# Optimization experiments

Hardware: AMD Instinct MI355X
Metric: run time of the kernel (lower is better)

Reference implementation:

```python
import jax, jax.numpy as jnp
import numpy as np

B, D, ATT, C = 256, 2048, 512, 1024
TEMP = 4.0  # cfg.JS_Softmax_Temp
SCALE = 20.0
N_GROUPS = 32


def setup_inputs() -> dict:
    key = jax.random.key(0)
    k1, k2, k3, k4 = jax.random.split(key, 4)
    x = jax.random.normal(k1, (B, D), dtype=jnp.float32)
    gt_s_labels = jax.random.randint(k2, (B,), 0, N_GROUPS)
    W = jax.random.normal(k3, (ATT, D), dtype=jnp.float32) * 0.02  # Linear weight [out,in]
    b = jnp.zeros((ATT,), dtype=jnp.float32)
    seen_att = jax.random.normal(k4, (C, ATT), dtype=jnp.float32)
    return {"x": x, "gt_s_labels": gt_s_labels, "W": W, "b": b, "seen_att": seen_att}


def _l2norm(v):
    return v / jnp.maximum(jnp.linalg.norm(v, axis=-1, keepdims=True), 1e-12)


def _adv_loss(x, W, b, seen_att, labels):
    # GRL is identity in forward; classifier = Linear(D, ATT)
    y_att = _l2norm(x @ W.T + b)            # [B, ATT]
    sa = _l2norm(seen_att)                   # [C, ATT]
    logits = SCALE * (y_att @ sa.T)          # [B, C]
    logP = jax.nn.log_softmax(logits / TEMP, axis=-1)
    P = jnp.exp(logP)                        # [B, C] softmax distributions
    # Pairwise mixture log((p_i + p_j)/2): [B, B, C]
    logM = jnp.log((P[:, None, :] + P[None, :, :]) * 0.5)
    negH = jnp.sum(P * logP, axis=-1)        # [B], = -entropy_i
    cross = jnp.einsum('ic,ijc->ij', P, logM)  # sum_c p_i log m_ij
    A = negH[:, None] - cross                # KL(p_i || m_ij), [B, B]
    JS = 0.5 * (A + A.T)                     # m symmetric => JS_ij
    idx = jnp.arange(B)
    mask = (labels[:, None] == labels[None, :]) & (idx[None, :] > idx[:, None])
    cnt = jnp.sum(mask)
    loss = jnp.where(cnt == 0, jnp.float32(0.0),
                     jnp.sum(jnp.where(mask, JS, 0.0)) / jnp.maximum(cnt, 1).astype(jnp.float32))
    return loss * (TEMP ** 2)


def reference(x, gt_s_labels, W, b, seen_att):
    return _adv_loss(x, W, b, seen_att, gt_s_labels)
```

## Files before the change

kernel.cpp:

```cpp
#include <hip/hip_runtime.h>
#include <math.h>

static constexpr int Bn  = 256;
static constexpr int Dd  = 2048;
static constexpr int ATT = 512;
static constexpr int Cc  = 1024;
static constexpr int SK1 = 16;
static constexpr int SK2 = 8;
static constexpr int BM = 128, BN = 64, BK = 32;
static constexpr int APITCH = BK + 8;

typedef __attribute__((ext_vector_type(8))) short short8v;
typedef __attribute__((ext_vector_type(4))) float f32x4;

__device__ __forceinline__ float wave_reduce_sum(float v) {
#pragma unroll
    for (int off = 32; off; off >>= 1) v += __shfl_down(v, off, 64);
    return v;
}
__device__ __forceinline__ float wave_reduce_max(float v) {
#pragma unroll
    for (int off = 32; off; off >>= 1) v = fmaxf(v, __shfl_down(v, off, 64));
    return v;
}
__device__ __forceinline__ float block_reduce_sum(float v) {
    __shared__ float sm_s[4];
    v = wave_reduce_sum(v);
    __syncthreads();
    if ((threadIdx.x & 63) == 0) sm_s[threadIdx.x >> 6] = v;
    __syncthreads();
    return sm_s[0] + sm_s[1] + sm_s[2] + sm_s[3];
}
__device__ __forceinline__ float block_reduce_max(float v) {
    __shared__ float sm_m[4];
    v = wave_reduce_max(v);
    __syncthreads();
    if ((threadIdx.x & 63) == 0) sm_m[threadIdx.x >> 6] = v;
    __syncthreads();
    return fmaxf(fmaxf(sm_m[0], sm_m[1]), fmaxf(sm_m[2], sm_m[3]));
}

__device__ __forceinline__ void splitbf(float v, unsigned short& h, unsigned short& l) {
    const unsigned int b = __float_as_uint(v);
    h = (unsigned short)(b >> 16);
    const float r = v - __uint_as_float(b & 0xFFFF0000u);
    l = (unsigned short)(__float_as_uint(r) >> 16);
}
__device__ __forceinline__ void stage4(const float4 v, unsigned short* hi,
                                       unsigned short* lo, int off) {
    unsigned short h0, h1, h2, h3, l0, l1, l2, l3;
    splitbf(v.x, h0, l0); splitbf(v.y, h1, l1);
    splitbf(v.z, h2, l2); splitbf(v.w, h3, l3);
    *(ushort4*)(hi + off) = make_ushort4(h0, h1, h2, h3);
    *(ushort4*)(lo + off) = make_ushort4(l0, l1, l2, l3);
}

__device__ __forceinline__ void gemm_tile_mfma(const float* __restrict__ A,
                                               const float* __restrict__ B,
                                               float* __restrict__ dst, int N, int K,
                                               int row0, int col0, int kbase, int kc,
                                               unsigned short* __restrict__ Ahi,
                                               unsigned short* __restrict__ Alo,
                                               unsigned short* __restrict__ Bhi,
                                               unsigned short* __restrict__ Blo) {
    constexpr int FA = BK / 4;
    constexpr int NA = BM * FA / 256;
    constexpr int NB = BN * FA / 256;
    const int tid = threadIdx.x;
    const int lane = tid & 63, wv = tid >> 6;
    const int fr = lane & 15, fg = lane >> 4;

    float4 pa[NA], pb[NB];
#pragma unroll
    for (int u = 0; u < NA; ++u) {
        const int t = tid + u * 256, r = t / FA, c4 = (t % FA) * 4;
        pa[u] = *(const float4*)(A + (size_t)(row0 + r) * K + kbase + c4);
    }
#pragma unroll
    for (int u = 0; u < NB; ++u) {
        const int t = tid + u * 256, r = t / FA, c4 = (t % FA) * 4;
        pb[u] = *(const float4*)(B + (size_t)(col0 + r) * K + kbase + c4);
    }
    f32x4 acc[2][4] = {};
    for (int k0 = kbase; k0 < kbase + kc; k0 += BK) {
        __syncthreads();
#pragma unroll
        for (int u = 0; u < NA; ++u) {
            const int t = tid + u * 256, r = t / FA, c4 = (t % FA) * 4;
            stage4(pa[u], Ahi, Alo, r * APITCH + c4);
        }
#pragma unroll
        for (int u = 0; u < NB; ++u) {
            const int t = tid + u * 256, r = t / FA, c4 = (t % FA) * 4;
            stage4(pb[u], Bhi, Blo, r * APITCH + c4);
        }
        __syncthreads();
        if (k0 + BK < kbase + kc) {
            const int kn = k0 + BK;
#pragma unroll
            for (int u = 0; u < NA; ++u) {
                const int t = tid + u * 256, r = t / FA, c4 = (t % FA) * 4;
                pa[u] = *(const float4*)(A + (size_t)(row0 + r) * K + kn + c4);
            }
#pragma unroll
            for (int u = 0; u < NB; ++u) {
                const int t = tid + u * 256, r = t / FA, c4 = (t % FA) * 4;
                pb[u] = *(const float4*)(B + (size_t)(col0 + r) * K + kn + c4);
            }
        }
        short8v ah[2], al[2];
#pragma unroll
        for (int im = 0; im < 2; ++im) {
            const int mrow = (wv * 2 + im) * 16 + fr;
            ah[im] = *(short8v*)(Ahi + mrow * APITCH + fg * 8);
            al[im] = *(short8v*)(Alo + mrow * APITCH + fg * 8);
        }
#pragma unroll
        for (int in = 0; in < 4; ++in) {
            const int nrow = in * 16 + fr;
            const short8v bh = *(short8v*)(Bhi + nrow * APITCH + fg * 8);
            const short8v bl = *(short8v*)(Blo + nrow * APITCH + fg * 8);
#pragma unroll
            for (int im = 0; im < 2; ++im) {
                acc[im][in] = __builtin_amdgcn_mfma_f32_16x16x32_bf16(ah[im], bh, acc[im][in], 0, 0, 0);
                acc[im][in] = __builtin_amdgcn_mfma_f32_16x16x32_bf16(ah[im], bl, acc[im][in], 0, 0, 0);
                acc[im][in] = __builtin_amdgcn_mfma_f32_16x16x32_bf16(al[im], bh, acc[im][in], 0, 0, 0);
            }
        }
    }
#pragma unroll
    for (int im = 0; im < 2; ++im) {
#pragma unroll
        for (int in = 0; in < 4; ++in) {
#pragma unroll
            for (int r = 0; r < 4; ++r) {
                const int m = row0 + (wv * 2 + im) * 16 + fg * 4 + r;
                const int c = col0 + in * 16 + fr;
                dst[(size_t)m * N + c] = acc[im][in][r];
            }
        }
    }
}

__global__ __launch_bounds__(256, 2) void k1_gemm1_sanorm(const float* __restrict__ x,
                                                          const float* __restrict__ W,
                                                          const float* __restrict__ seen,
                                                          float* __restrict__ part,
                                                          float* __restrict__ sa,
                                                          int* __restrict__ doneCnt) {
    __shared__ unsigned short AhiS[BM * APITCH];
    __shared__ unsigned short AloS[BM * APITCH];
    __shared__ unsigned short BhiS[BN * APITCH];
    __shared__ unsigned short BloS[BN * APITCH];
    const int bid = blockIdx.x, tid = threadIdx.x;
    if (bid < 256) {
        const int bx = bid & 7, by = (bid >> 3) & 1, bz = bid >> 4;
        gemm_tile_mfma(x, W, part + (size_t)bz * Bn * ATT, ATT, Dd,
                       by * BM, bx * BN, bz * (Dd / SK1), Dd / SK1,
                       AhiS, AloS, BhiS, BloS);
    } else {
        if (bid == 256 && tid == 0) *doneCnt = 0;
#pragma unroll
        for (int u = 0; u < 4; ++u) {
            const int r = (bid - 256) * 4 + u, c = tid * 2;
            const float2 v = *(const float2*)(seen + (size_t)r * ATT + c);
            float ss = block_reduce_sum(fmaf(v.x, v.x, v.y * v.y));
            const float sc = 1.0f / fmaxf(sqrtf(ss), 1e-12f);
            *(float2*)(sa + (size_t)r * ATT + c) = make_float2(v.x * sc, v.y * sc);
        }
    }
}

__global__ __launch_bounds__(256) void k2_yanorm(const float* __restrict__ part,
                                                 const float* __restrict__ bias,
                                                 float* __restrict__ ya) {
    const int m = blockIdx.x, c = threadIdx.x * 2;
    float2 s = *(const float2*)(bias + c);
#pragma unroll
    for (int z = 0; z < SK1; ++z) {
        const float2 p = *(const float2*)(part + (size_t)z * Bn * ATT + (size_t)m * ATT + c);
        s.x += p.x; s.y += p.y;
    }
    float ss = block_reduce_sum(fmaf(s.x, s.x, s.y * s.y));
    const float sc = 1.0f / fmaxf(sqrtf(ss), 1e-12f);
    *(float2*)(ya + (size_t)m * ATT + c) = make_float2(s.x * sc, s.y * sc);
}

__global__ __launch_bounds__(256, 2) void k3_gemm2(const float* __restrict__ ya,
                                                   const float* __restrict__ sa,
                                                   float* __restrict__ part) {
    __shared__ unsigned short AhiS[BM * APITCH];
    __shared__ unsigned short AloS[BM * APITCH];
    __shared__ unsigned short BhiS[BN * APITCH];
    __shared__ unsigned short BloS[BN * APITCH];
    const int bid = blockIdx.x;
    const int bx = bid & 15, by = (bid >> 4) & 1, bz = bid >> 5;
    gemm_tile_mfma(ya, sa, part + (size_t)bz * Bn * Cc, Cc, ATT,
                   by * BM, bx * BN, bz * (ATT / SK2), ATT / SK2,
                   AhiS, AloS, BhiS, BloS);
}

__global__ __launch_bounds__(256) void k4_softmax(const float* __restrict__ part,
                                                  float* __restrict__ P,
                                                  float* __restrict__ negH) {
    const int i = blockIdx.x, c = threadIdx.x * 4;
    float4 a = make_float4(0.f, 0.f, 0.f, 0.f);
#pragma unroll
    for (int z = 0; z < SK2; ++z) {
        const float4 p = *(const float4*)(part + (size_t)z * Bn * Cc + (size_t)i * Cc + c);
        a.x += p.x; a.y += p.y; a.z += p.z; a.w += p.w;
    }
    float lv[4] = {a.x * 5.0f, a.y * 5.0f, a.z * 5.0f, a.w * 5.0f};
    float lm = fmaxf(fmaxf(lv[0], lv[1]), fmaxf(lv[2], lv[3]));
    lm = block_reduce_max(lm);
    float se = 0.f;
#pragma unroll
    for (int k = 0; k < 4; ++k) se += __expf(lv[k] - lm);
    se = block_reduce_sum(se);
    const float logZ = __logf(se);
    float nh = 0.f;
    float4 pv;
#pragma unroll
    for (int k = 0; k < 4; ++k) {
        const float lp = lv[k] - lm - logZ;
        const float p = __expf(lp);
        (&pv.x)[k] = p;
        nh = fmaf(p, lp, nh);
    }
    *(float4*)(P + (size_t)i * Cc + c) = pv;
    nh = block_reduce_sum(nh);
    if (threadIdx.x == 0) negH[i] = nh;
}

__global__ __launch_bounds__(256) void k5_pairjs_fin(const float* __restrict__ P,
                                                     const float* __restrict__ negH,
                                                     const int* __restrict__ labels,
                                                     float* __restrict__ pairSum,
                                                     float* __restrict__ pairCnt,
                                                     int* __restrict__ doneCnt,
                                                     float* __restrict__ out) {
    const int i = blockIdx.x, tid = threadIdx.x;
    __shared__ int lbl[Bn];
    __shared__ float nh_s[Bn];
    __shared__ int isLast;
    lbl[tid] = labels[tid];
    nh_s[tid] = negH[tid];
    __syncthreads();
    const int li = lbl[i];
    const float4 pi = *(const float4*)(P + (size_t)i * Cc + tid * 4);
    const float nhi = nh_s[i];

    float tsum = 0.f;
    float nsum = 0.f, cnt = 0.f;
    for (int j = i + 1; j < Bn; ++j) {
        if (lbl[j] != li) continue;
        const float4 pj = *(const float4*)(P + (size_t)j * Cc + tid * 4);
        float t;
        t = pi.x + pj.x; tsum = fmaf(t, __logf(0.5f * t), tsum);
        t = pi.y + pj.y; tsum = fmaf(t, __logf(0.5f * t), tsum);
        t = pi.z + pj.z; tsum = fmaf(t, __logf(0.5f * t), tsum);
        t = pi.w + pj.w; tsum = fmaf(t, __logf(0.5f * t), tsum);
        if (tid == 0) { nsum += nhi + nh_s[j]; cnt += 1.0f; }
    }
    const float s = block_reduce_sum(tsum);
    if (tid == 0) {
        pairSum[i] = 0.5f * (nsum - s);
        pairCnt[i] = cnt;
        __threadfence();
        isLast = (atomicAdd(doneCnt, 1) == Bn - 1);
    }
    __syncthreads();
    if (isLast) {
        __threadfence();
        float fs = block_reduce_sum(pairSum[tid]);
        __syncthreads();
        const float fc = block_reduce_sum(pairCnt[tid]);
        if (tid == 0) out[0] = (fc == 0.0f) ? 0.0f : (fs / fc) * 16.0f;
    }
}

extern "C" void kernel_launch(void* const* d_in, const int* in_sizes, int n_in,
                              void* d_out, int out_size, void* d_ws, size_t ws_size,
                              hipStream_t stream) {
    const float* x      = (const float*)d_in[0];
    const int*   labels = (const int*)d_in[1];
    const float* W      = (const float*)d_in[2];
    const float* bias   = (const float*)d_in[3];
    const float* seen   = (const float*)d_in[4];
    float* out = (float*)d_out;

    char* ws = (char*)d_ws;
    float* part    = (float*)(ws);
    float* sa      = (float*)(ws + (8u << 20));
    float* ya      = (float*)(ws + (10u << 20));
    float* P       = (float*)(ws + (10u << 20) + (512u << 10));
    float* negH    = (float*)(ws + (11u << 20) + (512u << 10));
    float* pairSum = negH + Bn;
    float* pairCnt = pairSum + Bn;
    int*   doneCnt = (int*)(pairCnt + Bn);

    k1_gemm1_sanorm<<<512, 256, 0, stream>>>(x, W, seen, part, sa, doneCnt);
    k2_yanorm<<<Bn, 256, 0, stream>>>(part, bias, ya);
    k3_gemm2<<<256, 256, 0, stream>>>(ya, sa, part);
    k4_softmax<<<Bn, 256, 0, stream>>>(part, P, negH);
    k5_pairjs_fin<<<Bn, 256, 0, stream>>>(P, negH, labels, pairSum, pairCnt, doneCnt, out);
}
```

Measured before the change: 51.39 us.

## Pre-split GEMM operands into bf16 hi/lo arrays and halve split-K factors

Adds a separate kernel that splits x and W into bf16 high and low halves once in global memory. The normalization kernels now write bf16 hi/lo pairs directly, so the GEMM tiles load ready-made bf16 data with 16-byte loads instead of converting fp32 inside every tile. Split-K factors are halved, which shrinks the grids and the partial-sum traffic but gives each block a longer K loop. The trade-off is an extra kernel launch and an extra pass over x and W to produce the split copies.

Result: slower. 55.85 us (+8.7%).

```diff
diff --git a/kernel.cpp b/kernel.cpp
--- a/kernel.cpp
+++ b/kernel.cpp
@@ -5,10 +5,10 @@
 static constexpr int Dd  = 2048;
 static constexpr int ATT = 512;
 static constexpr int Cc  = 1024;
-static constexpr int SK1 = 16;
-static constexpr int SK2 = 8;
+static constexpr int SK1 = 8;
+static constexpr int SK2 = 4;
 static constexpr int BM = 128, BN = 64, BK = 32;
-static constexpr int APITCH = BK + 8;
+static constexpr int AP = 40;
 
 typedef __attribute__((ext_vector_type(8))) short short8v;
 typedef __attribute__((ext_vector_type(4))) float f32x4;
@@ -46,80 +46,76 @@
     const float r = v - __uint_as_float(b & 0xFFFF0000u);
     l = (unsigned short)(__float_as_uint(r) >> 16);
 }
-__device__ __forceinline__ void stage4(const float4 v, unsigned short* hi,
-                                       unsigned short* lo, int off) {
+
+__global__ __launch_bounds__(256) void k0_split(const float* __restrict__ x,
+                                                const float* __restrict__ W,
+                                                unsigned short* __restrict__ xh,
+                                                unsigned short* __restrict__ xl,
+                                                unsigned short* __restrict__ wh,
+                                                unsigned short* __restrict__ wl) {
+    const float* src; unsigned short *dh, *dl; int idx;
+    if (blockIdx.x < 512) {
+        src = x; dh = xh; dl = xl; idx = blockIdx.x * 256 + threadIdx.x;
+    } else {
+        src = W; dh = wh; dl = wl; idx = (blockIdx.x - 512) * 256 + threadIdx.x;
+    }
+    const float4 v = ((const float4*)src)[idx];
     unsigned short h0, h1, h2, h3, l0, l1, l2, l3;
     splitbf(v.x, h0, l0); splitbf(v.y, h1, l1);
     splitbf(v.z, h2, l2); splitbf(v.w, h3, l3);
-    *(ushort4*)(hi + off) = make_ushort4(h0, h1, h2, h3);
-    *(ushort4*)(lo + off) = make_ushort4(l0, l1, l2, l3);
-}
-
-__device__ __forceinline__ void gemm_tile_mfma(const float* __restrict__ A,
-                                               const float* __restrict__ B,
-                                               float* __restrict__ dst, int N, int K,
-                                               int row0, int col0, int kbase, int kc,
-                                               unsigned short* __restrict__ Ahi,
-                                               unsigned short* __restrict__ Alo,
-                                               unsigned short* __restrict__ Bhi,
-                                               unsigned short* __restrict__ Blo) {
-    constexpr int FA = BK / 4;
-    constexpr int NA = BM * FA / 256;
-    constexpr int NB = BN * FA / 256;
+    *(ushort4*)(dh + (size_t)idx * 4) = make_ushort4(h0, h1, h2, h3);
+    *(ushort4*)(dl + (size_t)idx * 4) = make_ushort4(l0, l1, l2, l3);
+}
+
+__device__ __forceinline__ void gemm_tile_bf(const unsigned short* __restrict__ Ah,
+                                             const unsigned short* __restrict__ Al,
+                                             const unsigned short* __restrict__ Bh,
+                                             const unsigned short* __restrict__ Bl,
+                                             float* __restrict__ dst, int N, int K,
+                                             int row0, int col0, int kbase, int kc,
+                                             unsigned short* __restrict__ LAh,
+                                             unsigned short* __restrict__ LAl,
+                                             unsigned short* __restrict__ LBh,
+                                             unsigned short* __restrict__ LBl) {
     const int tid = threadIdx.x;
     const int lane = tid & 63, wv = tid >> 6;
     const int fr = lane & 15, fg = lane >> 4;
-
-    float4 pa[NA], pb[NB];
-#pragma unroll
-    for (int u = 0; u < NA; ++u) {
-        const int t = tid + u * 256, r = t / FA, c4 = (t % FA) * 4;
-        pa[u] = *(const float4*)(A + (size_t)(row0 + r) * K + kbase + c4);
-    }
-#pragma unroll
-    for (int u = 0; u < NB; ++u) {
-        const int t = tid + u * 256, r = t / FA, c4 = (t % FA) * 4;
-        pb[u] = *(const float4*)(B + (size_t)(col0 + r) * K + kbase + c4);
-    }
+    const int ar = tid >> 2, ac8 = (tid & 3) * 8;
+
+    short8v pah0, pah1, pal0, pal1, pbh0, pbl0;
+    #define LDG(p, r, kk) (*(const short8v*)((p) + (size_t)(r) * K + (kk)))
+    pah0 = LDG(Ah, row0 + ar, kbase + ac8);  pah1 = LDG(Ah, row0 + 64 + ar, kbase + ac8);
+    pal0 = LDG(Al, row0 + ar, kbase + ac8);  pal1 = LDG(Al, row0 + 64 + ar, kbase + ac8);
+    pbh0 = LDG(Bh, col0 + ar, kbase + ac8);  pbl0 = LDG(Bl, col0 + ar, kbase + ac8);
+
     f32x4 acc[2][4] = {};
     for (int k0 = kbase; k0 < kbase + kc; k0 += BK) {
         __syncthreads();
-#pragma unroll
-        for (int u = 0; u < NA; ++u) {
-            const int t = tid + u * 256, r = t / FA, c4 = (t % FA) * 4;
-            stage4(pa[u], Ahi, Alo, r * APITCH + c4);
-        }
-#pragma unroll
-        for (int u = 0; u < NB; ++u) {
-            const int t = tid + u * 256, r = t / FA, c4 = (t % FA) * 4;
-            stage4(pb[u], Bhi, Blo, r * APITCH + c4);
-        }
+        *(short8v*)(LAh + ar * AP + ac8) = pah0;
+        *(short8v*)(LAh + (64 + ar) * AP + ac8) = pah1;
+        *(short8v*)(LAl + ar * AP + ac8) = pal0;
+        *(short8v*)(LAl + (64 + ar) * AP + ac8) = pal1;
+        *(short8v*)(LBh + ar * AP + ac8) = pbh0;
+        *(short8v*)(LBl + ar * AP + ac8) = pbl0;
         __syncthreads();
         if (k0 + BK < kbase + kc) {
-            const int kn = k0 + BK;
-#pragma unroll
-            for (int u = 0; u < NA; ++u) {
-                const int t = tid + u * 256, r = t / FA, c4 = (t % FA) * 4;
-                pa[u] = *(const float4*)(A + (size_t)(row0 + r) * K + kn + c4);
-            }
-#pragma unroll
-            for (int u = 0; u < NB; ++u) {
-                const int t = tid + u * 256, r = t / FA, c4 = (t % FA) * 4;
-                pb[u] = *(const float4*)(B + (size_t)(col0 + r) * K + kn + c4);
-            }
+            const int kn = k0 + BK + ac8;
+            pah0 = LDG(Ah, row0 + ar, kn);  pah1 = LDG(Ah, row0 + 64 + ar, kn);
+            pal0 = LDG(Al, row0 + ar, kn);  pal1 = LDG(Al, row0 + 64 + ar, kn);
+            pbh0 = LDG(Bh, col0 + ar, kn);  pbl0 = LDG(Bl, col0 + ar, kn);
         }
         short8v ah[2], al[2];
 #pragma unroll
         for (int im = 0; im < 2; ++im) {
             const int mrow = (wv * 2 + im) * 16 + fr;
-            ah[im] = *(short8v*)(Ahi + mrow * APITCH + fg * 8);
-            al[im] = *(short8v*)(Alo + mrow * APITCH + fg * 8);
+            ah[im] = *(short8v*)(LAh + mrow * AP + fg * 8);
+            al[im] = *(short8v*)(LAl + mrow * AP + fg * 8);
         }
 #pragma unroll
         for (int in = 0; in < 4; ++in) {
             const int nrow = in * 16 + fr;
-            const short8v bh = *(short8v*)(Bhi + nrow * APITCH + fg * 8);
-            const short8v bl = *(short8v*)(Blo + nrow * APITCH + fg * 8);
+            const short8v bh = *(short8v*)(LBh + nrow * AP + fg * 8);
+            const short8v bl = *(short8v*)(LBl + nrow * AP + fg * 8);
 #pragma unroll
             for (int im = 0; im < 2; ++im) {
                 acc[im][in] = __builtin_amdgcn_mfma_f32_16x16x32_bf16(ah[im], bh, acc[im][in], 0, 0, 0);
@@ -128,52 +124,55 @@
             }
         }
     }
-#pragma unroll
-    for (int im = 0; im < 2; ++im) {
-#pragma unroll
-        for (int in = 0; in < 4; ++in) {
+    #undef LDG
+#pragma unroll
+    for (int im = 0; im < 2; ++im)
+#pragma unroll
+        for (int in = 0; in < 4; ++in)
 #pragma unroll
             for (int r = 0; r < 4; ++r) {
                 const int m = row0 + (wv * 2 + im) * 16 + fg * 4 + r;
                 const int c = col0 + in * 16 + fr;
                 dst[(size_t)m * N + c] = acc[im][in][r];
             }
-        }
-    }
-}
-
-__global__ __launch_bounds__(256, 2) void k1_gemm1_sanorm(const float* __restrict__ x,
-                                                          const float* __restrict__ W,
+}
+
+__global__ __launch_bounds__(256, 2) void k1_gemm1_sanorm(const unsigned short* __restrict__ xh,
+                                                          const unsigned short* __restrict__ xl,
+                                                          const unsigned short* __restrict__ wh,
+                                                          const unsigned short* __restrict__ wl,
                                                           const float* __restrict__ seen,
                                                           float* __restrict__ part,
-                                                          float* __restrict__ sa,
+                                                          unsigned short* __restrict__ sah,
+                                                          unsigned short* __restrict__ sal,
                                                           int* __restrict__ doneCnt) {
-    __shared__ unsigned short AhiS[BM * APITCH];
-    __shared__ unsigned short AloS[BM * APITCH];
-    __shared__ unsigned short BhiS[BN * APITCH];
-    __shared__ unsigned short BloS[BN * APITCH];
+    __shared__ unsigned short LAh[BM * AP], LAl[BM * AP];
+    __shared__ unsigned short LBh[BN * AP], LBl[BN * AP];
     const int bid = blockIdx.x, tid = threadIdx.x;
-    if (bid < 256) {
+    if (bid < 128) {
         const int bx = bid & 7, by = (bid >> 3) & 1, bz = bid >> 4;
-        gemm_tile_mfma(x, W, part + (size_t)bz * Bn * ATT, ATT, Dd,
-                       by * BM, bx * BN, bz * (Dd / SK1), Dd / SK1,
-                       AhiS, AloS, BhiS, BloS);
+        gemm_tile_bf(xh, xl, wh, wl, part + (size_t)bz * Bn * ATT, ATT, Dd,
+                     by * BM, bx * BN, bz * (Dd / SK1), Dd / SK1, LAh, LAl, LBh, LBl);
     } else {
-        if (bid == 256 && tid == 0) *doneCnt = 0;
+        if (bid == 128 && tid == 0) *doneCnt = 0;
 #pragma unroll
         for (int u = 0; u < 4; ++u) {
-            const int r = (bid - 256) * 4 + u, c = tid * 2;
+            const int r = (bid - 128) * 4 + u, c = tid * 2;
             const float2 v = *(const float2*)(seen + (size_t)r * ATT + c);
             float ss = block_reduce_sum(fmaf(v.x, v.x, v.y * v.y));
             const float sc = 1.0f / fmaxf(sqrtf(ss), 1e-12f);
-            *(float2*)(sa + (size_t)r * ATT + c) = make_float2(v.x * sc, v.y * sc);
+            unsigned short h0, h1, l0, l1;
+            splitbf(v.x * sc, h0, l0); splitbf(v.y * sc, h1, l1);
+            *(ushort2*)(sah + (size_t)r * ATT + c) = make_ushort2(h0, h1);
+            *(ushort2*)(sal + (size_t)r * ATT + c) = make_ushort2(l0, l1);
         }
     }
 }
 
 __global__ __launch_bounds__(256) void k2_yanorm(const float* __restrict__ part,
                                                  const float* __restrict__ bias,
-                                                 float* __restrict__ ya) {
+                                                 unsigned short* __restrict__ yah,
+                                                 unsigned short* __restrict__ yal) {
     const int m = blockIdx.x, c = threadIdx.x * 2;
     float2 s = *(const float2*)(bias + c);
 #pragma unroll
@@ -183,21 +182,23 @@
     }
     float ss = block_reduce_sum(fmaf(s.x, s.x, s.y * s.y));
     const float sc = 1.0f / fmaxf(sqrtf(ss), 1e-12f);
-    *(float2*)(ya + (size_t)m * ATT + c) = make_float2(s.x * sc, s.y * sc);
-}
-
-__global__ __launch_bounds__(256, 2) void k3_gemm2(const float* __restrict__ ya,
-                                                   const float* __restrict__ sa,
+    unsigned short h0, h1, l0, l1;
+    splitbf(s.x * sc, h0, l0); splitbf(s.y * sc, h1, l1);
+    *(ushort2*)(yah + (size_t)m * ATT + c) = make_ushort2(h0, h1);
+    *(ushort2*)(yal + (size_t)m * ATT + c) = make_ushort2(l0, l1);
+}
+
+__global__ __launch_bounds__(256, 2) void k3_gemm2(const unsigned short* __restrict__ yah,
+                                                   const unsigned short* __restrict__ yal,
+                                                   const unsigned short* __restrict__ sah,
+                                                   const unsigned short* __restrict__ sal,
                                                    float* __restrict__ part) {
-    __shared__ unsigned short AhiS[BM * APITCH];
-    __shared__ unsigned short AloS[BM * APITCH];
-    __shared__ unsigned short BhiS[BN * APITCH];
-    __shared__ unsigned short BloS[BN * APITCH];
+    __shared__ unsigned short LAh[BM * AP], LAl[BM * AP];
+    __shared__ unsigned short LBh[BN * AP], LBl[BN * AP];
     const int bid = blockIdx.x;
     const int bx = bid & 15, by = (bid >> 4) & 1, bz = bid >> 5;
-    gemm_tile_mfma(ya, sa, part + (size_t)bz * Bn * Cc, Cc, ATT,
-                   by * BM, bx * BN, bz * (ATT / SK2), ATT / SK2,
-                   AhiS, AloS, BhiS, BloS);
+    gemm_tile_bf(yah, yal, sah, sal, part + (size_t)bz * Bn * Cc, Cc, ATT,
+                 by * BM, bx * BN, bz * (ATT / SK2), ATT / SK2, LAh, LAl, LBh, LBl);
 }
 
 __global__ __launch_bounds__(256) void k4_softmax(const float* __restrict__ part,
@@ -290,18 +291,25 @@
     float* out = (float*)d_out;
 
     char* ws = (char*)d_ws;
-    float* part    = (float*)(ws);
-    float* sa      = (float*)(ws + (8u << 20));
-    float* ya      = (float*)(ws + (10u << 20));
-    float* P       = (float*)(ws + (10u << 20) + (512u << 10));
-    float* negH    = (float*)(ws + (11u << 20) + (512u << 10));
+    float*          part = (float*)(ws);
+    unsigned short* xh   = (unsigned short*)(ws + (4u << 20));
+    unsigned short* xl   = (unsigned short*)(ws + (5u << 20));
+    unsigned short* wh   = (unsigned short*)(ws + (6u << 20));
+    unsigned short* wl   = (unsigned short*)(ws + (8u << 20));
+    unsigned short* sah  = (unsigned short*)(ws + (10u << 20));
+    unsigned short* sal  = (unsigned short*)(ws + (11u << 20));
+    unsigned short* yah  = (unsigned short*)(ws + (12u << 20));
+    unsigned short* yal  = (unsigned short*)(ws + (12u << 20) + (256u << 10));
+    float*          P    = (float*)(ws + (13u << 20));
+    float*          negH = (float*)(ws + (14u << 20));
     float* pairSum = negH + Bn;
     float* pairCnt = pairSum + Bn;
     int*   doneCnt = (int*)(pairCnt + Bn);
 
-    k1_gemm1_sanorm<<<512, 256, 0, stream>>>(x, W, seen, part, sa, doneCnt);
-    k2_yanorm<<<Bn, 256, 0, stream>>>(part, bias, ya);
-    k3_gemm2<<<256, 256, 0, stream>>>(ya, sa, part);
+    k0_split<<<1536, 256, 0, stream>>>(x, W, xh, xl, wh, wl);
+    k1_gemm1_sanorm<<<384, 256, 0, stream>>>(xh, xl, wh, wl, seen, part, sah, sal, doneCnt);
+    k2_yanorm<<<Bn, 256, 0, stream>>>(part, bias, yah, yal);
+    k3_gemm2<<<128, 256, 0, stream>>>(yah, yal, sah, sal, part);
     k4_softmax<<<Bn, 256, 0, stream>>>(part, P, negH);
     k5_pairjs_fin<<<Bn, 256, 0, stream>>>(P, negH, labels, pairSum, pairCnt, doneCnt, out);
 }
```

## Fuse y-norm into GEMM1 and softmax into pair-JS via grid-wide spin barriers

Applied to the files above, without the earlier changes.

Removes two kernel launches. The y_att normalization now runs in the sa-norm blocks of the first kernel after they spin on a counter bumped by the GEMM tiles. Softmax now runs at the start of the pair-JS kernel, followed by a grid-wide atomic barrier. A hipMemsetAsync resets the counters each call. This cuts launch gaps between stages, but it depends on all blocks being co-resident to avoid deadlock and adds a memset plus spin-wait overhead.

New measurement: 156.0 us. 204% more time.

```diff
diff --git a/kernel.cpp b/kernel.cpp
--- a/kernel.cpp
+++ b/kernel.cpp
@@ -8,7 +8,7 @@
 static constexpr int SK1 = 16;
 static constexpr int SK2 = 8;
 static constexpr int BM = 128, BN = 64, BK = 32;
-static constexpr int APITCH = BK + 8;
+static constexpr int APITCH = 40;
 
 typedef __attribute__((ext_vector_type(8))) short short8v;
 typedef __attribute__((ext_vector_type(4))) float f32x4;
@@ -38,6 +38,19 @@
     if ((threadIdx.x & 63) == 0) sm_m[threadIdx.x >> 6] = v;
     __syncthreads();
     return fmaxf(fmaxf(sm_m[0], sm_m[1]), fmaxf(sm_m[2], sm_m[3]));
+}
+
+__device__ __forceinline__ void signal_done(int* cnt) {
+    __threadfence();
+    if (threadIdx.x == 0) atomicAdd(cnt, 1);
+}
+__device__ __forceinline__ void wait_for(int* cnt, int target) {
+    if (threadIdx.x == 0) {
+        while (__hip_atomic_load(cnt, __ATOMIC_ACQUIRE, __HIP_MEMORY_SCOPE_AGENT) < target)
+            __builtin_amdgcn_s_sleep(2);
+    }
+    __syncthreads();
+    __threadfence();
 }
 
 __device__ __forceinline__ void splitbf(float v, unsigned short& h, unsigned short& l) {
@@ -129,25 +142,25 @@
         }
     }
 #pragma unroll
-    for (int im = 0; im < 2; ++im) {
-#pragma unroll
-        for (int in = 0; in < 4; ++in) {
+    for (int im = 0; im < 2; ++im)
+#pragma unroll
+        for (int in = 0; in < 4; ++in)
 #pragma unroll
             for (int r = 0; r < 4; ++r) {
                 const int m = row0 + (wv * 2 + im) * 16 + fg * 4 + r;
                 const int c = col0 + in * 16 + fr;
                 dst[(size_t)m * N + c] = acc[im][in][r];
             }
-        }
-    }
-}
-
-__global__ __launch_bounds__(256, 2) void k1_gemm1_sanorm(const float* __restrict__ x,
-                                                          const float* __restrict__ W,
-                                                          const float* __restrict__ seen,
-                                                          float* __restrict__ part,
-                                                          float* __restrict__ sa,
-                                                          int* __restrict__ doneCnt) {
+}
+
+__global__ __launch_bounds__(256, 2) void k1_gemm1_norms(const float* __restrict__ x,
+                                                         const float* __restrict__ W,
+                                                         const float* __restrict__ seen,
+                                                         const float* __restrict__ bias,
+                                                         float* __restrict__ part,
+                                                         float* __restrict__ sa,
+                                                         float* __restrict__ ya,
+                                                         int* __restrict__ g1done) {
     __shared__ unsigned short AhiS[BM * APITCH];
     __shared__ unsigned short AloS[BM * APITCH];
     __shared__ unsigned short BhiS[BN * APITCH];
@@ -158,8 +171,9 @@
         gemm_tile_mfma(x, W, part + (size_t)bz * Bn * ATT, ATT, Dd,
                        by * BM, bx * BN, bz * (Dd / SK1), Dd / SK1,
                        AhiS, AloS, BhiS, BloS);
+        __syncthreads();
+        signal_done(g1done);
     } else {
-        if (bid == 256 && tid == 0) *doneCnt = 0;
 #pragma unroll
         for (int u = 0; u < 4; ++u) {
             const int r = (bid - 256) * 4 + u, c = tid * 2;
@@ -168,22 +182,18 @@
             const float sc = 1.0f / fmaxf(sqrtf(ss), 1e-12f);
             *(float2*)(sa + (size_t)r * ATT + c) = make_float2(v.x * sc, v.y * sc);
         }
-    }
-}
-
-__global__ __launch_bounds__(256) void k2_yanorm(const float* __restrict__ part,
-                                                 const float* __restrict__ bias,
-                                                 float* __restrict__ ya) {
-    const int m = blockIdx.x, c = threadIdx.x * 2;
-    float2 s = *(const float2*)(bias + c);
-#pragma unroll
-    for (int z = 0; z < SK1; ++z) {
-        const float2 p = *(const float2*)(part + (size_t)z * Bn * ATT + (size_t)m * ATT + c);
-        s.x += p.x; s.y += p.y;
-    }
-    float ss = block_reduce_sum(fmaf(s.x, s.x, s.y * s.y));
-    const float sc = 1.0f / fmaxf(sqrtf(ss), 1e-12f);
-    *(float2*)(ya + (size_t)m * ATT + c) = make_float2(s.x * sc, s.y * sc);
+        wait_for(g1done, 256);
+        const int m = bid - 256, c = tid * 2;
+        float2 s = *(const float2*)(bias + c);
+#pragma unroll
+        for (int z = 0; z < SK1; ++z) {
+            const float2 p = *(const float2*)(part + (size_t)z * Bn * ATT + (size_t)m * ATT + c);
+            s.x += p.x; s.y += p.y;
+        }
+        float ss = block_reduce_sum(fmaf(s.x, s.x, s.y * s.y));
+        const float sc = 1.0f / fmaxf(sqrtf(ss), 1e-12f);
+        *(float2*)(ya + (size_t)m * ATT + c) = make_float2(s.x * sc, s.y * sc);
+    }
 }
 
 __global__ __launch_bounds__(256, 2) void k3_gemm2(const float* __restrict__ ya,
@@ -200,49 +210,53 @@
                    AhiS, AloS, BhiS, BloS);
 }
 
-__global__ __launch_bounds__(256) void k4_softmax(const float* __restrict__ part,
-                                                  float* __restrict__ P,
-                                                  float* __restrict__ negH) {
-    const int i = blockIdx.x, c = threadIdx.x * 4;
-    float4 a = make_float4(0.f, 0.f, 0.f, 0.f);
-#pragma unroll
-    for (int z = 0; z < SK2; ++z) {
-        const float4 p = *(const float4*)(part + (size_t)z * Bn * Cc + (size_t)i * Cc + c);
-        a.x += p.x; a.y += p.y; a.z += p.z; a.w += p.w;
-    }
-    float lv[4] = {a.x * 5.0f, a.y * 5.0f, a.z * 5.0f, a.w * 5.0f};
-    float lm = fmaxf(fmaxf(lv[0], lv[1]), fmaxf(lv[2], lv[3]));
-    lm = block_reduce_max(lm);
-    float se = 0.f;
-#pragma unroll
-    for (int k = 0; k < 4; ++k) se += __expf(lv[k] - lm);
-    se = block_reduce_sum(se);
-    const float logZ = __logf(se);
-    float nh = 0.f;
-    float4 pv;
-#pragma unroll
-    for (int k = 0; k < 4; ++k) {
-        const float lp = lv[k] - lm - logZ;
-        const float p = __expf(lp);
-        (&pv.x)[k] = p;
-        nh = fmaf(p, lp, nh);
-    }
-    *(float4*)(P + (size_t)i * Cc + c) = pv;
-    nh = block_reduce_sum(nh);
-    if (threadIdx.x == 0) negH[i] = nh;
-}
-
-__global__ __launch_bounds__(256) void k5_pairjs_fin(const float* __restrict__ P,
-                                                     const float* __restrict__ negH,
-                                                     const int* __restrict__ labels,
-                                                     float* __restrict__ pairSum,
-                                                     float* __restrict__ pairCnt,
-                                                     int* __restrict__ doneCnt,
-                                                     float* __restrict__ out) {
+__global__ __launch_bounds__(256) void k5_sm_pairjs_fin(const float* __restrict__ part,
+                                                        const int* __restrict__ labels,
+                                                        float* __restrict__ P,
+                                                        float* __restrict__ negH,
+                                                        float* __restrict__ pairSum,
+                                                        float* __restrict__ pairCnt,
+                                                        int* __restrict__ smdone,
+                                                        int* __restrict__ jsdone,
+                                                        float* __restrict__ out) {
     const int i = blockIdx.x, tid = threadIdx.x;
     __shared__ int lbl[Bn];
     __shared__ float nh_s[Bn];
     __shared__ int isLast;
+
+    {
+        const int c = tid * 4;
+        float4 a = make_float4(0.f, 0.f, 0.f, 0.f);
+#pragma unroll
+        for (int z = 0; z < SK2; ++z) {
+            const float4 p = *(const float4*)(part + (size_t)z * Bn * Cc + (size_t)i * Cc + c);
+            a.x += p.x; a.y += p.y; a.z += p.z; a.w += p.w;
+        }
+        float lv[4] = {a.x * 5.0f, a.y * 5.0f, a.z * 5.0f, a.w * 5.0f};
+        float lm = fmaxf(fmaxf(lv[0], lv[1]), fmaxf(lv[2], lv[3]));
+        lm = block_reduce_max(lm);
+        float se = 0.f;
+#pragma unroll
+        for (int k = 0; k < 4; ++k) se += __expf(lv[k] - lm);
+        se = block_reduce_sum(se);
+        const float logZ = __logf(se);
+        float nh = 0.f;
+        float4 pv;
+#pragma unroll
+        for (int k = 0; k < 4; ++k) {
+            const float lp = lv[k] - lm - logZ;
+            const float p = __expf(lp);
+            (&pv.x)[k] = p;
+            nh = fmaf(p, lp, nh);
+        }
+        *(float4*)(P + (size_t)i * Cc + c) = pv;
+        nh = block_reduce_sum(nh);
+        if (tid == 0) negH[i] = nh;
+    }
+    __syncthreads();
+    signal_done(smdone);
+    wait_for(smdone, 256);
+
     lbl[tid] = labels[tid];
     nh_s[tid] = negH[tid];
     __syncthreads();
@@ -267,7 +281,7 @@
         pairSum[i] = 0.5f * (nsum - s);
         pairCnt[i] = cnt;
         __threadfence();
-        isLast = (atomicAdd(doneCnt, 1) == Bn - 1);
+        isLast = (atomicAdd(jsdone, 1) == Bn - 1);
     }
     __syncthreads();
     if (isLast) {
@@ -297,11 +311,11 @@
     float* negH    = (float*)(ws + (11u << 20) + (512u << 10));
     float* pairSum = negH + Bn;
     float* pairCnt = pairSum + Bn;
-    int*   doneCnt = (int*)(pairCnt + Bn);
-
-    k1_gemm1_sanorm<<<512, 256, 0, stream>>>(x, W, seen, part, sa, doneCnt);
-    k2_yanorm<<<Bn, 256, 0, stream>>>(part, bias, ya);
+    int*   ctrs    = (int*)(pairCnt + Bn);
+
+    hipMemsetAsync(ctrs, 0, 16, stream);
+    k1_gemm1_norms<<<512, 256, 0, stream>>>(x, W, seen, bias, part, sa, ya, ctrs + 0);
     k3_gemm2<<<256, 256, 0, stream>>>(ya, sa, part);
-    k4_softmax<<<Bn, 256, 0, stream>>>(part, P, negH);
-    k5_pairjs_fin<<<Bn, 256, 0, stream>>>(P, negH, labels, pairSum, pairCnt, doneCnt, out);
-}
+    k5_sm_pairjs_fin<<<Bn, 256, 0, stream>>>(part, labels, P, negH, pairSum, pairCnt,
+                                             ctrs + 1, ctrs + 2, out);
+}
```

## Fuse softmax and pairwise JS into per-label-group kernel with LDS-cached rows

Applied to the files above, without the earlier changes.

Replaces the per-row softmax kernel and the per-row pairwise JS kernel with one kernel that launches one block per label group. Each block gathers its group's rows, computes their softmax serially, and keeps up to 20 probability rows in shared memory for the pairwise mixture-entropy loop. Rows beyond that spill to a global buffer. This drops one kernel launch and the global round trip for P, and it skips scanning rows of other labels. The cost is parallelism: only 32 blocks run, each doing serial per-row block reductions, and large groups add latency. The code also assumes labels lie in [0,32).

New measurement: 93.18 us. 1.81x slower.

```diff
diff --git a/kernel.cpp b/kernel.cpp
--- a/kernel.cpp
+++ b/kernel.cpp
@@ -5,10 +5,12 @@
 static constexpr int Dd  = 2048;
 static constexpr int ATT = 512;
 static constexpr int Cc  = 1024;
+static constexpr int NG  = 32;
+static constexpr int CAP = 20;
 static constexpr int SK1 = 16;
 static constexpr int SK2 = 8;
 static constexpr int BM = 128, BN = 64, BK = 32;
-static constexpr int APITCH = BK + 8;
+static constexpr int APITCH = 40;
 
 typedef __attribute__((ext_vector_type(8))) short short8v;
 typedef __attribute__((ext_vector_type(4))) float f32x4;
@@ -129,17 +131,15 @@
         }
     }
 #pragma unroll
-    for (int im = 0; im < 2; ++im) {
-#pragma unroll
-        for (int in = 0; in < 4; ++in) {
+    for (int im = 0; im < 2; ++im)
+#pragma unroll
+        for (int in = 0; in < 4; ++in)
 #pragma unroll
             for (int r = 0; r < 4; ++r) {
                 const int m = row0 + (wv * 2 + im) * 16 + fg * 4 + r;
                 const int c = col0 + in * 16 + fr;
                 dst[(size_t)m * N + c] = acc[im][in][r];
             }
-        }
-    }
 }
 
 __global__ __launch_bounds__(256, 2) void k1_gemm1_sanorm(const float* __restrict__ x,
@@ -200,81 +200,94 @@
                    AhiS, AloS, BhiS, BloS);
 }
 
-__global__ __launch_bounds__(256) void k4_softmax(const float* __restrict__ part,
-                                                  float* __restrict__ P,
-                                                  float* __restrict__ negH) {
-    const int i = blockIdx.x, c = threadIdx.x * 4;
-    float4 a = make_float4(0.f, 0.f, 0.f, 0.f);
-#pragma unroll
-    for (int z = 0; z < SK2; ++z) {
-        const float4 p = *(const float4*)(part + (size_t)z * Bn * Cc + (size_t)i * Cc + c);
-        a.x += p.x; a.y += p.y; a.z += p.z; a.w += p.w;
-    }
-    float lv[4] = {a.x * 5.0f, a.y * 5.0f, a.z * 5.0f, a.w * 5.0f};
-    float lm = fmaxf(fmaxf(lv[0], lv[1]), fmaxf(lv[2], lv[3]));
-    lm = block_reduce_max(lm);
-    float se = 0.f;
-#pragma unroll
-    for (int k = 0; k < 4; ++k) se += __expf(lv[k] - lm);
-    se = block_reduce_sum(se);
-    const float logZ = __logf(se);
-    float nh = 0.f;
-    float4 pv;
-#pragma unroll
-    for (int k = 0; k < 4; ++k) {
-        const float lp = lv[k] - lm - logZ;
-        const float p = __expf(lp);
-        (&pv.x)[k] = p;
-        nh = fmaf(p, lp, nh);
-    }
-    *(float4*)(P + (size_t)i * Cc + c) = pv;
-    nh = block_reduce_sum(nh);
-    if (threadIdx.x == 0) negH[i] = nh;
-}
-
-__global__ __launch_bounds__(256) void k5_pairjs_fin(const float* __restrict__ P,
-                                                     const float* __restrict__ negH,
-                                                     const int* __restrict__ labels,
-                                                     float* __restrict__ pairSum,
-                                                     float* __restrict__ pairCnt,
-                                                     int* __restrict__ doneCnt,
-                                                     float* __restrict__ out) {
-    const int i = blockIdx.x, tid = threadIdx.x;
-    __shared__ int lbl[Bn];
+__global__ __launch_bounds__(256) void k45_group_js(const float* __restrict__ part,
+                                                    const int* __restrict__ labels,
+                                                    float* __restrict__ Pglob,
+                                                    float* __restrict__ gSum,
+                                                    float* __restrict__ gCnt,
+                                                    int* __restrict__ doneCnt,
+                                                    float* __restrict__ out) {
+    const int g = blockIdx.x, tid = threadIdx.x;
+    __shared__ float Psm[CAP][Cc];
     __shared__ float nh_s[Bn];
-    __shared__ int isLast;
-    lbl[tid] = labels[tid];
-    nh_s[tid] = negH[tid];
-    __syncthreads();
-    const int li = lbl[i];
-    const float4 pi = *(const float4*)(P + (size_t)i * Cc + tid * 4);
-    const float nhi = nh_s[i];
+    __shared__ int   rows[Bn];
+    __shared__ int   lblS[Bn];
+    __shared__ int   ng_s;
+    __shared__ int   isLast;
+
+    lblS[tid] = labels[tid];
+    __syncthreads();
+    if (tid == 0) {
+        int n = 0;
+        for (int j = 0; j < Bn; ++j)
+            if (lblS[j] == g) rows[n++] = j;
+        ng_s = n;
+    }
+    __syncthreads();
+    const int ng = ng_s;
+
+    const int c = tid * 4;
+    for (int idx = 0; idx < ng; ++idx) {
+        const int i = rows[idx];
+        float4 a = make_float4(0.f, 0.f, 0.f, 0.f);
+#pragma unroll
+        for (int z = 0; z < SK2; ++z) {
+            const float4 p = *(const float4*)(part + (size_t)z * Bn * Cc + (size_t)i * Cc + c);
+            a.x += p.x; a.y += p.y; a.z += p.z; a.w += p.w;
+        }
+        float lv[4] = {a.x * 5.0f, a.y * 5.0f, a.z * 5.0f, a.w * 5.0f};
+        float lm = fmaxf(fmaxf(lv[0], lv[1]), fmaxf(lv[2], lv[3]));
+        lm = block_reduce_max(lm);
+        float se = 0.f;
+#pragma unroll
+        for (int k = 0; k < 4; ++k) se += __expf(lv[k] - lm);
+        se = block_reduce_sum(se);
+        const float logZ = __logf(se);
+        float nh = 0.f;
+        float4 pv;
+#pragma unroll
+        for (int k = 0; k < 4; ++k) {
+            const float lp = lv[k] - lm - logZ;
+            const float p = __expf(lp);
+            (&pv.x)[k] = p;
+            nh = fmaf(p, lp, nh);
+        }
+        if (idx < CAP) *(float4*)(&Psm[idx][c]) = pv;
+        else           *(float4*)(Pglob + (size_t)i * Cc + c) = pv;
+        nh = block_reduce_sum(nh);
+        if (tid == 0) nh_s[idx] = nh;
+    }
+    __syncthreads();
 
     float tsum = 0.f;
     float nsum = 0.f, cnt = 0.f;
-    for (int j = i + 1; j < Bn; ++j) {
-        if (lbl[j] != li) continue;
-        const float4 pj = *(const float4*)(P + (size_t)j * Cc + tid * 4);
-        float t;
-        t = pi.x + pj.x; tsum = fmaf(t, __logf(0.5f * t), tsum);
-        t = pi.y + pj.y; tsum = fmaf(t, __logf(0.5f * t), tsum);
-        t = pi.z + pj.z; tsum = fmaf(t, __logf(0.5f * t), tsum);
-        t = pi.w + pj.w; tsum = fmaf(t, __logf(0.5f * t), tsum);
-        if (tid == 0) { nsum += nhi + nh_s[j]; cnt += 1.0f; }
+    for (int a2 = 0; a2 < ng; ++a2) {
+        const float4 pa = (a2 < CAP) ? *(const float4*)(&Psm[a2][c])
+                                     : *(const float4*)(Pglob + (size_t)rows[a2] * Cc + c);
+        for (int b2 = a2 + 1; b2 < ng; ++b2) {
+            const float4 pb = (b2 < CAP) ? *(const float4*)(&Psm[b2][c])
+                                         : *(const float4*)(Pglob + (size_t)rows[b2] * Cc + c);
+            float t;
+            t = pa.x + pb.x; tsum = fmaf(t, __logf(0.5f * t), tsum);
+            t = pa.y + pb.y; tsum = fmaf(t, __logf(0.5f * t), tsum);
+            t = pa.z + pb.z; tsum = fmaf(t, __logf(0.5f * t), tsum);
+            t = pa.w + pb.w; tsum = fmaf(t, __logf(0.5f * t), tsum);
+            if (tid == 0) { nsum += nh_s[a2] + nh_s[b2]; cnt += 1.0f; }
+        }
     }
     const float s = block_reduce_sum(tsum);
     if (tid == 0) {
-        pairSum[i] = 0.5f * (nsum - s);
-        pairCnt[i] = cnt;
+        gSum[g] = 0.5f * (nsum - s);
+        gCnt[g] = cnt;
         __threadfence();
-        isLast = (atomicAdd(doneCnt, 1) == Bn - 1);
+        isLast = (atomicAdd(doneCnt, 1) == NG - 1);
     }
     __syncthreads();
     if (isLast) {
         __threadfence();
-        float fs = block_reduce_sum(pairSum[tid]);
+        float fs = block_reduce_sum((tid < NG) ? gSum[tid] : 0.0f);
         __syncthreads();
-        const float fc = block_reduce_sum(pairCnt[tid]);
+        const float fc = block_reduce_sum((tid < NG) ? gCnt[tid] : 0.0f);
         if (tid == 0) out[0] = (fc == 0.0f) ? 0.0f : (fs / fc) * 16.0f;
     }
 }
@@ -293,15 +306,13 @@
     float* part    = (float*)(ws);
     float* sa      = (float*)(ws + (8u << 20));
     float* ya      = (float*)(ws + (10u << 20));
-    float* P       = (float*)(ws + (10u << 20) + (512u << 10));
-    float* negH    = (float*)(ws + (11u << 20) + (512u << 10));
-    float* pairSum = negH + Bn;
-    float* pairCnt = pairSum + Bn;
-    int*   doneCnt = (int*)(pairCnt + Bn);
+    float* Pglob   = (float*)(ws + (10u << 20) + (512u << 10));
+    float* gSum    = (float*)(ws + (11u << 20) + (512u << 10));
+    float* gCnt    = gSum + NG;
+    int*   doneCnt = (int*)(gCnt + NG);
 
     k1_gemm1_sanorm<<<512, 256, 0, stream>>>(x, W, seen, part, sa, doneCnt);
     k2_yanorm<<<Bn, 256, 0, stream>>>(part, bias, ya);
     k3_gemm2<<<256, 256, 0, stream>>>(ya, sa, part);
-    k4_softmax<<<Bn, 256, 0, stream>>>(part, P, negH);
-    k5_pairjs_fin<<<Bn, 256, 0, stream>>>(P, negH, labels, pairSum, pairCnt, doneCnt, out);
-}
+    k45_group_js<<<NG, 256, 0, stream>>>(part, labels, Pglob, gSum, gCnt, doneCnt, out);
+}
```
